# Performance work log

Hardware: AMD Instinct MI355X
Metric: run time of the kernel (lower is better)

## Reference

```python
import jax, jax.numpy as jnp
import numpy as np

B, S, D, H, DFF, V, LAT, L = 64, 256, 512, 8, 2048, 128, 512, 6
MAXLEN = 256
NEG = -1e9
EPS = 1e-5


def setup_inputs() -> dict:
    key = jax.random.key(0)
    ks = jax.random.split(key, 32)
    s = 0.02
    rn = lambda k, shape: jax.random.normal(k, shape, jnp.float32) * s
    inp = {
        "z": jax.random.normal(ks[0], (B, LAT), jnp.float32),
        "tgt_seq": jax.random.randint(ks[1], (B, S), 0, V),
        "emb": rn(ks[2], (V, D)).at[0].set(0.0),  # padding_idx=0 row zeroed
        "pos": rn(ks[3], (MAXLEN, D)),
        "proj_w": rn(ks[4], (D, LAT)),
        "proj_b": jnp.zeros((D,), jnp.float32),
        "sa_w": rn(ks[5], (L, 3 * D, D)),
        "sa_b": jnp.zeros((L, 3 * D), jnp.float32),
        "sa_ow": rn(ks[6], (L, D, D)),
        "sa_ob": jnp.zeros((L, D), jnp.float32),
        "ca_w": rn(ks[7], (L, 3 * D, D)),
        "ca_b": jnp.zeros((L, 3 * D), jnp.float32),
        "ca_ow": rn(ks[8], (L, D, D)),
        "ca_ob": jnp.zeros((L, D), jnp.float32),
        "ln1_s": jnp.ones((L, D), jnp.float32),
        "ln1_b": jnp.zeros((L, D), jnp.float32),
        "ln2_s": jnp.ones((L, D), jnp.float32),
        "ln2_b": jnp.zeros((L, D), jnp.float32),
        "ln3_s": jnp.ones((L, D), jnp.float32),
        "ln3_b": jnp.zeros((L, D), jnp.float32),
        "ff1_w": rn(ks[9], (L, DFF, D)),
        "ff1_b": jnp.zeros((L, DFF), jnp.float32),
        "ff2_w": rn(ks[10], (L, D, DFF)),
        "ff2_b": jnp.zeros((L, D), jnp.float32),
        "fc_w": rn(ks[11], (V, D)),
        "fc_b": jnp.zeros((V,), jnp.float32),
    }
    return inp


def _ln(x, s, b):
    m = jnp.mean(x, -1, keepdims=True)
    v = jnp.mean(jnp.square(x - m), -1, keepdims=True)
    return (x - m) * jax.lax.rsqrt(v + EPS) * s + b


def _mha(q_in, k_in, v_in, w, b, ow, ob, mask=None):
    # torch MultiheadAttention: packed in_proj [3D, D], out_proj [D, D]
    wq, wk, wv = w[:D], w[D:2 * D], w[2 * D:]
    bq, bk, bv = b[:D], b[D:2 * D], b[2 * D:]
    dh = D // H
    split = lambda t: t.reshape(t.shape[0], t.shape[1], H, dh)
    q = split(q_in @ wq.T + bq)  # [B,Sq,H,dh]
    k = split(k_in @ wk.T + bk)  # [B,Sk,H,dh]
    v = split(v_in @ wv.T + bv)
    scores = jnp.einsum("bqhd,bkhd->bhqk", q, k) / np.sqrt(dh).astype(np.float32)
    if mask is not None:
        scores = scores + mask
    attn = jax.nn.softmax(scores, axis=-1)
    out = jnp.einsum("bhqk,bkhd->bqhd", attn, v).reshape(q_in.shape[0], q_in.shape[1], D)
    return out @ ow.T + ob


def reference(z, tgt_seq, emb, pos, proj_w, proj_b, sa_w, sa_b, sa_ow, sa_ob,
              ca_w, ca_b, ca_ow, ca_ob, ln1_s, ln1_b, ln2_s, ln2_b, ln3_s, ln3_b,
              ff1_w, ff1_b, ff2_w, ff2_b, fc_w, fc_b):
    # memory = proj(z), length-1 cross-attention memory: [B,1,D]
    mem = (z @ proj_w.T + proj_b)[:, None, :]
    seq_len = tgt_seq.shape[1]
    x = emb[tgt_seq] + pos[:seq_len][None]  # [B,S,D]
    causal = jnp.where(jnp.tril(jnp.ones((seq_len, seq_len), bool)), 0.0, NEG)
    for i in range(L):  # post-norm TransformerDecoderLayer (torch default)
        sa = _mha(x, x, x, sa_w[i], sa_b[i], sa_ow[i], sa_ob[i], causal)
        x = _ln(x + sa, ln1_s[i], ln1_b[i])
        ca = _mha(x, mem, mem, ca_w[i], ca_b[i], ca_ow[i], ca_ob[i])
        x = _ln(x + ca, ln2_s[i], ln2_b[i])
        ff = jax.nn.relu(x @ ff1_w[i].T + ff1_b[i]) @ ff2_w[i].T + ff2_b[i]
        x = _ln(x + ff, ln3_s[i], ln3_b[i])
    logits = x @ fc_w.T + fc_b  # [B,S,V]
    return logits
```

## Files before the change

### kernel.cpp

```cpp
#include <hip/hip_runtime.h>

typedef unsigned int uint;
typedef unsigned short ushort;

typedef __attribute__((ext_vector_type(8))) __bf16 bf16x8;
typedef __attribute__((ext_vector_type(4))) float f32x4;

#define B_ 64
#define S_ 256
#define D_ 512
#define H_ 8
#define DFF_ 2048
#define V_ 128
#define L_ 6
#define BS_ (B_ * S_)

__device__ __forceinline__ float blo(uint u) { return __uint_as_float(u << 16); }
__device__ __forceinline__ float bhi(uint u) { return __uint_as_float(u & 0xffff0000u); }
__device__ __forceinline__ float b2f(ushort u) { return __uint_as_float(((uint)u) << 16); }
__device__ __forceinline__ ushort f2b(float f) {
  uint u = __float_as_uint(f);
  return (ushort)((u + 0x7fffu + ((u >> 16) & 1u)) >> 16);
}
__device__ __forceinline__ uint pack2(float a, float b) {
  return (uint)f2b(a) | ((uint)f2b(b) << 16);
}

#define GLOAD16(gp, lp)                                                        \
  __builtin_amdgcn_global_load_lds(                                            \
      (const __attribute__((address_space(1))) void*)(gp),                     \
      (__attribute__((address_space(3))) void*)(lp), 16, 0, 0)

__global__ __launch_bounds__(256) void conv_kernel(const float* __restrict__ src,
                                                   ushort* __restrict__ dst) {
  size_t p = (size_t)blockIdx.x * 256 + threadIdx.x;
  float2 v = ((const float2*)src)[p];
  ((uint*)dst)[p] = pack2(v.x, v.y);
}

__global__ __launch_bounds__(256) void embed_kernel(
    const int* __restrict__ tgt, const float* __restrict__ emb,
    const float* __restrict__ pos, ushort* __restrict__ x16) {
  int p = blockIdx.x * 256 + threadIdx.x;
  int row = p >> 8;
  int d2 = p & 255;
  int s = row & (S_ - 1);
  int tok = tgt[row];
  float2 e = ((const float2*)emb)[tok * 256 + d2];
  float2 pp = ((const float2*)pos)[s * 256 + d2];
  ((uint*)x16)[p] = pack2(e.x + pp.x, e.y + pp.y);
}

template <int MODE>
__global__ __launch_bounds__(256) void gemm_bt(
    const ushort* __restrict__ A, const ushort* __restrict__ W,
    const float* __restrict__ bias, void* __restrict__ Cv, int N, int K,
    int As, int Ws, int Cs) {
  __shared__ ushort la[128 * 32];
  __shared__ ushort lb[128 * 32];
  const int tid = threadIdx.x;
  const int wv = tid >> 6, lane = tid & 63;

  const int nwg = gridDim.x * gridDim.y;
  int lid = blockIdx.x + gridDim.x * blockIdx.y;
  lid = (lid & 7) * (nwg >> 3) + (lid >> 3);
  const int bx = lid % gridDim.x;
  const int by = lid / gridDim.x;
  const int m0 = by << 7, n0 = bx << 7;

  const int wm = (wv >> 1) << 6, wn = (wv & 1) << 6;
  const int tr = lane & 15, tq = lane >> 4;

  const int lin0 = wv * 1024 + lane * 8;
  const int lin1 = lin0 + 512;
  const int am0 = lin0 >> 5, ac0 = lin0 & 31;
  const int am1 = lin1 >> 5, ac1 = lin1 & 31;

  const ushort* pa0 = A + (size_t)(m0 + am0) * As + ac0;
  const ushort* pa1 = A + (size_t)(m0 + am1) * As + ac1;
  const ushort* pb0 = W + (size_t)(n0 + am0) * Ws + ac0;
  const ushort* pb1 = W + (size_t)(n0 + am1) * Ws + ac1;
  ushort* la0 = &la[wv * 1024];
  ushort* la1 = &la[wv * 1024 + 512];
  ushort* lb0 = &lb[wv * 1024];
  ushort* lb1 = &lb[wv * 1024 + 512];

  f32x4 acc[4][4];
#pragma unroll
  for (int i = 0; i < 4; ++i)
#pragma unroll
    for (int j = 0; j < 4; ++j) acc[i][j] = (f32x4)(0.f);

  const int KT = K >> 5;
  for (int kt = 0; kt < KT; ++kt) {
    const int kb = kt << 5;
    GLOAD16(pa0 + kb, la0);
    GLOAD16(pa1 + kb, la1);
    GLOAD16(pb0 + kb, lb0);
    GLOAD16(pb1 + kb, lb1);
    __syncthreads();
    bf16x8 av[4], bv[4];
#pragma unroll
    for (int i = 0; i < 4; ++i)
      av[i] = *(const bf16x8*)&la[(wm + i * 16 + tr) * 32 + tq * 8];
#pragma unroll
    for (int j = 0; j < 4; ++j)
      bv[j] = *(const bf16x8*)&lb[(wn + j * 16 + tr) * 32 + tq * 8];
#pragma unroll
    for (int i = 0; i < 4; ++i)
#pragma unroll
      for (int j = 0; j < 4; ++j)
        acc[i][j] =
            __builtin_amdgcn_mfma_f32_16x16x32_bf16(av[i], bv[j], acc[i][j], 0, 0, 0);
    __syncthreads();
  }

#pragma unroll
  for (int j = 0; j < 4; ++j) {
    const int gn = n0 + wn + j * 16 + tr;
    float bj = 0.f;
    if (MODE != 2) bj = bias[gn];
    float scl = 1.f;
    if (MODE == 4) scl = (gn < 512) ? 0.18033688011112042f : 1.f;
#pragma unroll
    for (int i = 0; i < 4; ++i) {
      const int gmb = m0 + wm + i * 16 + tq * 4;
#pragma unroll
      for (int r = 0; r < 4; ++r) {
        const size_t idx = (size_t)(gmb + r) * Cs + gn;
        float v = acc[i][j][r] + bj;
        if (MODE == 1) v = fmaxf(v, 0.f);
        if (MODE == 4) v *= scl;
        if (MODE == 3)
          ((float*)Cv)[idx] = v;
        else if (MODE == 2) {
          ushort* C = (ushort*)Cv;
          C[idx] = f2b(b2f(C[idx]) + acc[i][j][r]);
        } else
          ((ushort*)Cv)[idx] = f2b(v);
      }
    }
  }
}

__global__ __launch_bounds__(256) void gemm_btf(
    const ushort* __restrict__ A0, long zA, const float* __restrict__ W0,
    long zW, const float* __restrict__ bias0, long zb, ushort* __restrict__ C0,
    long zC, int N, int K, int As, int Ws, int Cs) {
  const int zz = blockIdx.z;
  const ushort* A = A0 + zA * zz;
  const float* W = W0 + zW * zz;
  const float* bias = bias0 + zb * zz;
  ushort* C = C0 + zC * zz;

  __shared__ ushort la[128 * 32];
  __shared__ ushort lb[128 * 32];
  const int tid = threadIdx.x;
  const int wv = tid >> 6, lane = tid & 63;
  const int m0 = blockIdx.y << 7, n0 = blockIdx.x << 7;
  const int wm = (wv >> 1) << 6, wn = (wv & 1) << 6;
  const int tr = lane & 15, tq = lane >> 4;

  const int lin0 = wv * 1024 + lane * 8;
  const int lin1 = lin0 + 512;
  const int am0 = lin0 >> 5, ac0 = lin0 & 31;
  const int am1 = lin1 >> 5, ac1 = lin1 & 31;

  const ushort* pa0 = A + (size_t)(m0 + am0) * As + ac0;
  const ushort* pa1 = A + (size_t)(m0 + am1) * As + ac1;
  const float* pb0 = W + (size_t)(n0 + am0) * Ws + ac0;
  const float* pb1 = W + (size_t)(n0 + am1) * Ws + ac1;

  f32x4 acc[4][4];
#pragma unroll
  for (int i = 0; i < 4; ++i)
#pragma unroll
    for (int j = 0; j < 4; ++j) acc[i][j] = (f32x4)(0.f);

  const int KT = K >> 5;
  for (int kt = 0; kt < KT; ++kt) {
    const int kb = kt << 5;
    uint4 ra0 = *(const uint4*)(pa0 + kb);
    uint4 ra1 = *(const uint4*)(pa1 + kb);
    float4 f00 = *(const float4*)(pb0 + kb);
    float4 f01 = *(const float4*)(pb0 + kb + 4);
    float4 f10 = *(const float4*)(pb1 + kb);
    float4 f11 = *(const float4*)(pb1 + kb + 4);
    uint4 rb0 = make_uint4(pack2(f00.x, f00.y), pack2(f00.z, f00.w),
                           pack2(f01.x, f01.y), pack2(f01.z, f01.w));
    uint4 rb1 = make_uint4(pack2(f10.x, f10.y), pack2(f10.z, f10.w),
                           pack2(f11.x, f11.y), pack2(f11.z, f11.w));
    __syncthreads();
    *(uint4*)&la[lin0] = ra0;
    *(uint4*)&la[lin1] = ra1;
    *(uint4*)&lb[lin0] = rb0;
    *(uint4*)&lb[lin1] = rb1;
    __syncthreads();
    bf16x8 av[4], bv[4];
#pragma unroll
    for (int i = 0; i < 4; ++i)
      av[i] = *(const bf16x8*)&la[(wm + i * 16 + tr) * 32 + tq * 8];
#pragma unroll
    for (int j = 0; j < 4; ++j)
      bv[j] = *(const bf16x8*)&lb[(wn + j * 16 + tr) * 32 + tq * 8];
#pragma unroll
    for (int i = 0; i < 4; ++i)
#pragma unroll
      for (int j = 0; j < 4; ++j)
        acc[i][j] =
            __builtin_amdgcn_mfma_f32_16x16x32_bf16(av[i], bv[j], acc[i][j], 0, 0, 0);
  }

#pragma unroll
  for (int j = 0; j < 4; ++j) {
    const int gn = n0 + wn + j * 16 + tr;
    const float bj = bias[gn];
#pragma unroll
    for (int i = 0; i < 4; ++i) {
      const int gmb = m0 + wm + i * 16 + tq * 4;
#pragma unroll
      for (int r = 0; r < 4; ++r)
        C[(size_t)(gmb + r) * Cs + gn] = f2b(acc[i][j][r] + bj);
    }
  }
}

__global__ __launch_bounds__(128) void attn_mfma(ushort* __restrict__ qkv) {
  __shared__ ushort lk[64 * 72];
  __shared__ ushort lvT[64 * 72];
  __shared__ ushort lp[2 * 64 * 72];
  const int qp = blockIdx.x, h = blockIdx.y, b = blockIdx.z;
  const int tid = threadIdx.x;
  const int g = tid >> 6, lane = tid & 63;
  const int tr = lane & 15, tq = lane >> 4;
  const int qc = qp * 2 + g;
  const int q0 = qc << 6;
  ushort* myp = &lp[g * 64 * 72];

  bf16x8 qf[4][2];
#pragma unroll
  for (int i = 0; i < 4; ++i)
#pragma unroll
    for (int s = 0; s < 2; ++s)
      qf[i][s] = *(const bf16x8*)(qkv +
                                  (size_t)(b * 256 + q0 + i * 16 + tr) * 1536 +
                                  h * 64 + s * 32 + tq * 8);

  f32x4 o[4][4];
  float pl[4][4];
#pragma unroll
  for (int i = 0; i < 4; ++i)
#pragma unroll
    for (int j = 0; j < 4; ++j) {
      o[i][j] = (f32x4)(0.f);
      pl[i][j] = 0.f;
    }

  const int key = tid >> 1, half = tid & 1;
  const int cmax = qp * 2 + 1;
  for (int c = 0; c <= cmax; ++c) {
    __syncthreads();
    const ushort* gk =
        qkv + (size_t)(b * 256 + c * 64 + key) * 1536 + 512 + h * 64 + half * 32;
#pragma unroll
    for (int u = 0; u < 4; ++u)
      *(uint4*)&lk[key * 72 + half * 32 + u * 8] = *(const uint4*)(gk + u * 8);
    ushort vloc[32];
#pragma unroll
    for (int u = 0; u < 4; ++u)
      *(uint4*)&vloc[u * 8] = *(const uint4*)(gk + 512 + u * 8);
#pragma unroll
    for (int dd = 0; dd < 32; ++dd)
      lvT[(half * 32 + dd) * 72 + key] = vloc[dd];
    __syncthreads();

    if (c <= qc) {
      f32x4 Sv[4][4];
#pragma unroll
      for (int i = 0; i < 4; ++i)
#pragma unroll
        for (int j = 0; j < 4; ++j) Sv[i][j] = (f32x4)(0.f);
      bf16x8 kf[4][2];
#pragma unroll
      for (int j = 0; j < 4; ++j)
#pragma unroll
        for (int s = 0; s < 2; ++s)
          kf[j][s] = *(const bf16x8*)&lk[(j * 16 + tr) * 72 + s * 32 + tq * 8];
#pragma unroll
      for (int i = 0; i < 4; ++i)
#pragma unroll
        for (int j = 0; j < 4; ++j) {
          Sv[i][j] = __builtin_amdgcn_mfma_f32_16x16x32_bf16(qf[i][0], kf[j][0],
                                                             Sv[i][j], 0, 0, 0);
          Sv[i][j] = __builtin_amdgcn_mfma_f32_16x16x32_bf16(qf[i][1], kf[j][1],
                                                             Sv[i][j], 0, 0, 0);
        }
      const bool diag = (c == qc);
#pragma unroll
      for (int i = 0; i < 4; ++i)
#pragma unroll
        for (int j = 0; j < 4; ++j)
#pragma unroll
          for (int r = 0; r < 4; ++r) {
            float e = exp2f(Sv[i][j][r]);
            if (diag && (j * 16 + tr) > (i * 16 + tq * 4 + r)) e = 0.f;
            pl[i][r] += e;
            myp[(i * 16 + tq * 4 + r) * 72 + j * 16 + tr] =
                (ushort)(__float_as_uint(e) >> 16);
          }
#pragma unroll
      for (int s = 0; s < 2; ++s) {
        bf16x8 vf[4], af[4];
#pragma unroll
        for (int jn = 0; jn < 4; ++jn)
          vf[jn] = *(const bf16x8*)&lvT[(jn * 16 + tr) * 72 + s * 32 + tq * 8];
#pragma unroll
        for (int im = 0; im < 4; ++im)
          af[im] = *(const bf16x8*)&myp[(im * 16 + tr) * 72 + s * 32 + tq * 8];
#pragma unroll
        for (int im = 0; im < 4; ++im)
#pragma unroll
          for (int jn = 0; jn < 4; ++jn)
            o[im][jn] = __builtin_amdgcn_mfma_f32_16x16x32_bf16(af[im], vf[jn],
                                                                o[im][jn], 0, 0, 0);
      }
    }
  }

#pragma unroll
  for (int i = 0; i < 4; ++i)
#pragma unroll
    for (int r = 0; r < 4; ++r) {
      float v = pl[i][r];
      v += __shfl_xor(v, 1, 64);
      v += __shfl_xor(v, 2, 64);
      v += __shfl_xor(v, 4, 64);
      v += __shfl_xor(v, 8, 64);
      pl[i][r] = 1.f / v;
    }

#pragma unroll
  for (int i = 0; i < 4; ++i)
#pragma unroll
    for (int j = 0; j < 4; ++j)
#pragma unroll
      for (int r = 0; r < 4; ++r)
        qkv[(size_t)(b * 256 + q0 + i * 16 + tq * 4 + r) * 1536 + h * 64 +
            j * 16 + tr] = f2b(o[i][j][r] * pl[i][r]);
}

__global__ __launch_bounds__(256) void ln12_kernel(
    ushort* __restrict__ x16, const uint* __restrict__ d1,
    const uint* __restrict__ cavec, const float* __restrict__ s1,
    const float* __restrict__ b1, const float* __restrict__ s2,
    const float* __restrict__ b2p) {
  const int r = blockIdx.x, t = threadIdx.x;
  const int lane = t & 63, wv = t >> 6;
  uint* xr = (uint*)x16 + (size_t)r * 256;
  uint xu = xr[t];
  uint du = d1[(size_t)r * 768 + t];
  float v0 = blo(xu) + blo(du), v1 = bhi(xu) + bhi(du);
  __shared__ float redA[4][2], redB[4][2];
  float sm = v0 + v1, sq = v0 * v0 + v1 * v1;
#pragma unroll
  for (int o = 32; o > 0; o >>= 1) {
    sm += __shfl_xor(sm, o, 64);
    sq += __shfl_xor(sq, o, 64);
  }
  if (lane == 0) {
    redA[wv][0] = sm;
    redA[wv][1] = sq;
  }
  __syncthreads();
  sm = redA[0][0] + redA[1][0] + redA[2][0] + redA[3][0];
  sq = redA[0][1] + redA[1][1] + redA[2][1] + redA[3][1];
  float mean = sm * (1.f / 512.f);
  float var = sq * (1.f / 512.f) - mean * mean;
  float rs = rsqrtf(var + 1e-5f);
  float2 sa = ((const float2*)s1)[t];
  float2 ba = ((const float2*)b1)[t];
  uint cu = cavec[(size_t)(r >> 8) * 256 + t];
  float w0 = (v0 - mean) * rs * sa.x + ba.x + blo(cu);
  float w1 = (v1 - mean) * rs * sa.y + ba.y + bhi(cu);
  sm = w0 + w1;
  sq = w0 * w0 + w1 * w1;
#pragma unroll
  for (int o = 32; o > 0; o >>= 1) {
    sm += __shfl_xor(sm, o, 64);
    sq += __shfl_xor(sq, o, 64);
  }
  if (lane == 0) {
    redB[wv][0] = sm;
    redB[wv][1] = sq;
  }
  __syncthreads();
  sm = redB[0][0] + redB[1][0] + redB[2][0] + redB[3][0];
  sq = redB[0][1] + redB[1][1] + redB[2][1] + redB[3][1];
  mean = sm * (1.f / 512.f);
  var = sq * (1.f / 512.f) - mean * mean;
  rs = rsqrtf(var + 1e-5f);
  float2 sb = ((const float2*)s2)[t];
  float2 bb = ((const float2*)b2p)[t];
  float y0 = (w0 - mean) * rs * sb.x + bb.x;
  float y1 = (w1 - mean) * rs * sb.y + bb.y;
  xr[t] = pack2(y0, y1);
}

__global__ __launch_bounds__(256) void ln_kernel(
    ushort* __restrict__ x16, const uint* __restrict__ delta, int DsU,
    const float* __restrict__ sc, const float* __restrict__ bi) {
  const int r = blockIdx.x, t = threadIdx.x;
  const int lane = t & 63, wv = t >> 6;
  uint* xr = (uint*)x16 + (size_t)r * 256;
  uint xu = xr[t];
  uint du = delta[(size_t)r * DsU + t];
  float v0 = blo(xu) + blo(du), v1 = bhi(xu) + bhi(du);
  float sm = v0 + v1, sq = v0 * v0 + v1 * v1;
#pragma unroll
  for (int o = 32; o > 0; o >>= 1) {
    sm += __shfl_xor(sm, o, 64);
    sq += __shfl_xor(sq, o, 64);
  }
  __shared__ float red[4][2];
  if (lane == 0) {
    red[wv][0] = sm;
    red[wv][1] = sq;
  }
  __syncthreads();
  sm = red[0][0] + red[1][0] + red[2][0] + red[3][0];
  sq = red[0][1] + red[1][1] + red[2][1] + red[3][1];
  float mean = sm * (1.f / 512.f);
  float var = sq * (1.f / 512.f) - mean * mean;
  float rs = rsqrtf(var + 1e-5f);
  float2 s2 = ((const float2*)sc)[t];
  float2 b2 = ((const float2*)bi)[t];
  float y0 = (v0 - mean) * rs * s2.x + b2.x;
  float y1 = (v1 - mean) * rs * s2.y + b2.y;
  xr[t] = pack2(y0, y1);
}

extern "C" void kernel_launch(void* const* d_in, const int* in_sizes, int n_in,
                              void* d_out, int out_size, void* d_ws,
                              size_t ws_size, hipStream_t stream) {
  (void)in_sizes; (void)n_in; (void)out_size; (void)ws_size;
  const float* z = (const float*)d_in[0];
  const int* tgt = (const int*)d_in[1];
  const float* emb = (const float*)d_in[2];
  const float* pos = (const float*)d_in[3];
  const float* projw = (const float*)d_in[4];
  const float* projb = (const float*)d_in[5];
  const float* saw = (const float*)d_in[6];
  const float* sab = (const float*)d_in[7];
  const float* saow = (const float*)d_in[8];
  const float* saob = (const float*)d_in[9];
  const float* caw = (const float*)d_in[10];
  const float* cab = (const float*)d_in[11];
  const float* caow = (const float*)d_in[12];
  const float* caob = (const float*)d_in[13];
  const float* ln1s = (const float*)d_in[14];
  const float* ln1b = (const float*)d_in[15];
  const float* ln2s = (const float*)d_in[16];
  const float* ln2b = (const float*)d_in[17];
  const float* ln3s = (const float*)d_in[18];
  const float* ln3b = (const float*)d_in[19];
  const float* ff1w = (const float*)d_in[20];
  const float* ff1b = (const float*)d_in[21];
  const float* ff2w = (const float*)d_in[22];
  const float* ff2b = (const float*)d_in[23];
  const float* fcw = (const float*)d_in[24];
  const float* fcb = (const float*)d_in[25];

  char* w8 = (char*)d_ws;
  ushort* x16 = (ushort*)w8;
  ushort* qkv = (ushort*)(w8 + (16u << 20));
  ushort* hbuf = qkv;
  ushort* fdel = (ushort*)(w8 + (48u << 20));
  ushort* z16 = (ushort*)(w8 + (64u << 20));
  ushort* memv16 = z16 + 128 * 512;
  ushort* cav16 = memv16 + 128 * 512;
  ushort* cavec16 = cav16 + (size_t)L_ * 128 * 512;
  ushort* wsaw = (ushort*)(w8 + (66u << 20));
  ushort* wsaow = wsaw + (size_t)L_ * 1536 * 512;
  ushort* wff1 = wsaow + (size_t)L_ * 512 * 512;
  ushort* wff2 = wff1 + (size_t)L_ * 2048 * 512;
  ushort* wfcw = wff2 + (size_t)L_ * 512 * 2048;

  conv_kernel<<<(L_ * 1536 * 512) / 512, 256, 0, stream>>>(saw, wsaw);
  conv_kernel<<<(L_ * 512 * 512) / 512, 256, 0, stream>>>(saow, wsaow);
  conv_kernel<<<(L_ * 2048 * 512) / 512, 256, 0, stream>>>(ff1w, wff1);
  conv_kernel<<<(L_ * 512 * 2048) / 512, 256, 0, stream>>>(ff2w, wff2);
  conv_kernel<<<(V_ * 512) / 512, 256, 0, stream>>>(fcw, wfcw);
  conv_kernel<<<(B_ * 512) / 512, 256, 0, stream>>>(z, z16);

  embed_kernel<<<16384, 256, 0, stream>>>(tgt, emb, pos, x16);

  gemm_btf<<<dim3(4, 1, 1), 256, 0, stream>>>(z16, 0, projw, 0, projb, 0,
                                              memv16, 0, 512, 512, 512, 512, 512);
  gemm_btf<<<dim3(4, 1, L_), 256, 0, stream>>>(
      memv16, 0, caw + 1024 * 512, (long)1536 * 512, cab + 1024, 1536, cav16,
      (long)128 * 512, 512, 512, 512, 512, 512);
  gemm_btf<<<dim3(4, 1, L_), 256, 0, stream>>>(
      cav16, (long)128 * 512, caow, (long)512 * 512, caob, 512, cavec16,
      (long)128 * 512, 512, 512, 512, 512, 512);

  for (int i = 0; i < L_; ++i) {
    gemm_bt<4><<<dim3(12, 128), 256, 0, stream>>>(
        x16, wsaw + (size_t)i * 1536 * 512, sab + i * 1536, qkv, 1536, 512, 512,
        512, 1536);
    attn_mfma<<<dim3(2, H_, B_), 128, 0, stream>>>(qkv);
    gemm_bt<0><<<dim3(4, 128), 256, 0, stream>>>(
        qkv, wsaow + (size_t)i * 512 * 512, saob + i * 512, qkv + 512, 512, 512,
        1536, 512, 1536);
    ln12_kernel<<<16384, 256, 0, stream>>>(
        x16, (const uint*)(qkv + 512), (const uint*)(cavec16 + (size_t)i * 128 * 512),
        ln1s + i * 512, ln1b + i * 512, ln2s + i * 512, ln2b + i * 512);
    gemm_bt<1><<<dim3(8, 128), 256, 0, stream>>>(
        x16, wff1 + (size_t)i * 2048 * 512, ff1b + i * 2048, hbuf, 1024, 512,
        512, 512, 1024);
    gemm_bt<0><<<dim3(4, 128), 256, 0, stream>>>(
        hbuf, wff2 + (size_t)i * 512 * 2048, ff2b + i * 512, fdel, 512, 1024,
        1024, 2048, 512);
    gemm_bt<1><<<dim3(8, 128), 256, 0, stream>>>(
        x16, wff1 + ((size_t)i * 2048 + 1024) * 512, ff1b + i * 2048 + 1024,
        hbuf, 1024, 512, 512, 512, 1024);
    gemm_bt<2><<<dim3(4, 128), 256, 0, stream>>>(
        hbuf, wff2 + (size_t)i * 512 * 2048 + 1024, (const float*)0, fdel, 512,
        1024, 1024, 2048, 512);
    ln_kernel<<<16384, 256, 0, stream>>>(x16, (const uint*)fdel, 256,
                                         ln3s + i * 512, ln3b + i * 512);
  }
  gemm_bt<3><<<dim3(1, 128), 256, 0, stream>>>(x16, wfcw, fcb, d_out, 128, 512,
                                               512, 512, 128);
}
```

Measured before the change: 1.819 ms.

## Add double-buffered register-staged GEMM with 64-wide K tiles for decoder layers

Adds a new GEMM kernel that prefetches the next K tile from global memory into registers while MFMAs run on the current LDS buffer, then writes it into the alternate LDS buffer. Each step covers 64 K elements, so there are half as many barriers per output tile. All per-layer projection and FFN GEMMs switch to it. The cost is double the LDS (64KB per block) and more registers, which may reduce occupancy, and the LDS layout has no padding, so bank conflicts are possible.

```diff
diff --git a/kernel.cpp b/kernel.cpp
--- a/kernel.cpp
+++ b/kernel.cpp
@@ -49,6 +49,128 @@
   float2 e = ((const float2*)emb)[tok * 256 + d2];
   float2 pp = ((const float2*)pos)[s * 256 + d2];
   ((uint*)x16)[p] = pack2(e.x + pp.x, e.y + pp.y);
+}
+
+template <int MODE>
+__global__ __launch_bounds__(256) void gemm_rs(
+    const ushort* __restrict__ A, const ushort* __restrict__ W,
+    const float* __restrict__ bias, void* __restrict__ Cv, int N, int K,
+    int As, int Ws, int Cs) {
+  __shared__ ushort la[2][8192];
+  __shared__ ushort lb[2][8192];
+  const int tid = threadIdx.x;
+  const int wv = tid >> 6, lane = tid & 63;
+
+  const int nwg = gridDim.x * gridDim.y;
+  int lid = blockIdx.x + gridDim.x * blockIdx.y;
+  lid = (lid & 7) * (nwg >> 3) + (lid >> 3);
+  const int bx = lid % gridDim.x;
+  const int by = lid / gridDim.x;
+  const int m0 = by << 7, n0 = bx << 7;
+
+  const int wm = (wv >> 1) << 6, wn = (wv & 1) << 6;
+  const int tr = lane & 15, tq = lane >> 4;
+
+  const int lin0 = wv * 1024 + lane * 8;
+  const int am0 = lin0 >> 5, ac0 = lin0 & 31;
+  const int lin1 = lin0 + 512;
+  const int am1 = lin1 >> 5, ac1 = lin1 & 31;
+
+  const ushort* pa0 = A + (size_t)(m0 + am0) * As + ac0;
+  const ushort* pa1 = A + (size_t)(m0 + am1) * As + ac1;
+  const ushort* pb0 = W + (size_t)(n0 + am0) * Ws + ac0;
+  const ushort* pb1 = W + (size_t)(n0 + am1) * Ws + ac1;
+
+  f32x4 acc[4][4];
+#pragma unroll
+  for (int i = 0; i < 4; ++i)
+#pragma unroll
+    for (int j = 0; j < 4; ++j) acc[i][j] = (f32x4)(0.f);
+
+  const int KT = K >> 6;
+  uint4 ra0, ra1, ra2, ra3, rb0, rb1, rb2, rb3;
+
+#define LOADR(t)                                                               \
+  do {                                                                         \
+    const int kb_ = (t) << 6;                                                  \
+    ra0 = *(const uint4*)(pa0 + kb_);                                          \
+    ra1 = *(const uint4*)(pa1 + kb_);                                          \
+    ra2 = *(const uint4*)(pa0 + kb_ + 32);                                     \
+    ra3 = *(const uint4*)(pa1 + kb_ + 32);                                     \
+    rb0 = *(const uint4*)(pb0 + kb_);                                          \
+    rb1 = *(const uint4*)(pb1 + kb_);                                          \
+    rb2 = *(const uint4*)(pb0 + kb_ + 32);                                     \
+    rb3 = *(const uint4*)(pb1 + kb_ + 32);                                     \
+  } while (0)
+#define WRITR(d)                                                               \
+  do {                                                                         \
+    *(uint4*)&la[d][lin0] = ra0;                                               \
+    *(uint4*)&la[d][lin1] = ra1;                                               \
+    *(uint4*)&la[d][4096 + lin0] = ra2;                                        \
+    *(uint4*)&la[d][4096 + lin1] = ra3;                                        \
+    *(uint4*)&lb[d][lin0] = rb0;                                               \
+    *(uint4*)&lb[d][lin1] = rb1;                                               \
+    *(uint4*)&lb[d][4096 + lin0] = rb2;                                        \
+    *(uint4*)&lb[d][4096 + lin1] = rb3;                                        \
+  } while (0)
+
+  LOADR(0);
+  WRITR(0);
+  __syncthreads();
+
+  for (int t = 0; t < KT; ++t) {
+    const int d = t & 1;
+    if (t + 1 < KT) LOADR(t + 1);
+    bf16x8 av[2][4], bv[2][4];
+#pragma unroll
+    for (int s = 0; s < 2; ++s) {
+#pragma unroll
+      for (int i = 0; i < 4; ++i)
+        av[s][i] =
+            *(const bf16x8*)&la[d][s * 4096 + (wm + i * 16 + tr) * 32 + tq * 8];
+#pragma unroll
+      for (int j = 0; j < 4; ++j)
+        bv[s][j] =
+            *(const bf16x8*)&lb[d][s * 4096 + (wn + j * 16 + tr) * 32 + tq * 8];
+    }
+#pragma unroll
+    for (int s = 0; s < 2; ++s)
+#pragma unroll
+      for (int i = 0; i < 4; ++i)
+#pragma unroll
+        for (int j = 0; j < 4; ++j)
+          acc[i][j] = __builtin_amdgcn_mfma_f32_16x16x32_bf16(
+              av[s][i], bv[s][j], acc[i][j], 0, 0, 0);
+    if (t + 1 < KT) WRITR(d ^ 1);
+    __syncthreads();
+  }
+#undef LOADR
+#undef WRITR
+
+#pragma unroll
+  for (int j = 0; j < 4; ++j) {
+    const int gn = n0 + wn + j * 16 + tr;
+    float bj = 0.f;
+    if (MODE != 2) bj = bias[gn];
+    float scl = 1.f;
+    if (MODE == 4) scl = (gn < 512) ? 0.18033688011112042f : 1.f;
+#pragma unroll
+    for (int i = 0; i < 4; ++i) {
+      const int gmb = m0 + wm + i * 16 + tq * 4;
+#pragma unroll
+      for (int r = 0; r < 4; ++r) {
+        const size_t idx = (size_t)(gmb + r) * Cs + gn;
+        float v = acc[i][j][r] + bj;
+        if (MODE == 1) v = fmaxf(v, 0.f);
+        if (MODE == 4) v *= scl;
+        if (MODE == 2) {
+          ushort* C = (ushort*)Cv;
+          C[idx] = f2b(b2f(C[idx]) + acc[i][j][r]);
+        } else
+          ((ushort*)Cv)[idx] = f2b(v);
+      }
+    }
+  }
 }
 
 template <int MODE>
@@ -504,26 +626,26 @@
       (long)128 * 512, 512, 512, 512, 512, 512);
 
   for (int i = 0; i < L_; ++i) {
-    gemm_bt<4><<<dim3(12, 128), 256, 0, stream>>>(
+    gemm_rs<4><<<dim3(12, 128), 256, 0, stream>>>(
         x16, wsaw + (size_t)i * 1536 * 512, sab + i * 1536, qkv, 1536, 512, 512,
         512, 1536);
     attn_mfma<<<dim3(2, H_, B_), 128, 0, stream>>>(qkv);
-    gemm_bt<0><<<dim3(4, 128), 256, 0, stream>>>(
+    gemm_rs<0><<<dim3(4, 128), 256, 0, stream>>>(
         qkv, wsaow + (size_t)i * 512 * 512, saob + i * 512, qkv + 512, 512, 512,
         1536, 512, 1536);
     ln12_kernel<<<16384, 256, 0, stream>>>(
         x16, (const uint*)(qkv + 512), (const uint*)(cavec16 + (size_t)i * 128 * 512),
         ln1s + i * 512, ln1b + i * 512, ln2s + i * 512, ln2b + i * 512);
-    gemm_bt<1><<<dim3(8, 128), 256, 0, stream>>>(
+    gemm_rs<1><<<dim3(8, 128), 256, 0, stream>>>(
         x16, wff1 + (size_t)i * 2048 * 512, ff1b + i * 2048, hbuf, 1024, 512,
         512, 512, 1024);
-    gemm_bt<0><<<dim3(4, 128), 256, 0, stream>>>(
+    gemm_rs<0><<<dim3(4, 128), 256, 0, stream>>>(
         hbuf, wff2 + (size_t)i * 512 * 2048, ff2b + i * 512, fdel, 512, 1024,
         1024, 2048, 512);
-    gemm_bt<1><<<dim3(8, 128), 256, 0, stream>>>(
+    gemm_rs<1><<<dim3(8, 128), 256, 0, stream>>>(
         x16, wff1 + ((size_t)i * 2048 + 1024) * 512, ff1b + i * 2048 + 1024,
         hbuf, 1024, 512, 512, 512, 1024);
-    gemm_bt<2><<<dim3(4, 128), 256, 0, stream>>>(
+    gemm_rs<2><<<dim3(4, 128), 256, 0, stream>>>(
         hbuf, wff2 + (size_t)i * 512 * 2048 + 1024, (const float*)0, fdel, 512,
         1024, 1024, 2048, 512);
     ln_kernel<<<16384, 256, 0, stream>>>(x16, (const uint*)fdel, 256,
```

Result: faster. 1.612 ms (-11.4%).
